# Optimization experiments

Measured on AMD Instinct MI355X. Metric: run time of the kernel, lower is better.

The kernel has to match this reference:

```python
import jax, jax.numpy as jnp
import numpy as np

DIM = 768
N_HEADS = 12
HEAD_DIM = DIM // N_HEADS
SCALE = 1.0 / (DIM ** 0.5)  # NOTE: module divides by sqrt(dim), not sqrt(head_dim)


def setup_inputs() -> dict:
    key = jax.random.key(0)
    ks = jax.random.split(key, 9)
    B, N = 16, 1024
    std = 1.0 / np.sqrt(DIM)
    inputs = jax.random.normal(ks[0], (B, N, DIM), dtype=jnp.float32)
    Wq = jax.random.normal(ks[1], (DIM, DIM), dtype=jnp.float32) * std
    bq = jax.random.normal(ks[2], (DIM,), dtype=jnp.float32) * std
    Wk = jax.random.normal(ks[3], (DIM, DIM), dtype=jnp.float32) * std
    bk = jax.random.normal(ks[4], (DIM,), dtype=jnp.float32) * std
    Wv = jax.random.normal(ks[5], (DIM, DIM), dtype=jnp.float32) * std
    bv = jax.random.normal(ks[6], (DIM,), dtype=jnp.float32) * std
    Wo = jax.random.normal(ks[7], (DIM, DIM), dtype=jnp.float32) * std
    bo = jax.random.normal(ks[8], (DIM,), dtype=jnp.float32) * std
    return {"inputs": inputs, "Wq": Wq, "bq": bq, "Wk": Wk, "bk": bk,
            "Wv": Wv, "bv": bv, "Wo": Wo, "bo": bo}


def _split_heads(x, B, N):
    # [B, N, DIM] -> [B, H, N, hd]
    return x.reshape(B, N, N_HEADS, HEAD_DIM).transpose(0, 2, 1, 3)


def reference(inputs, Wq, bq, Wk, bk, Wv, bv, Wo, bo):
    B, N, _ = inputs.shape
    q = _split_heads(inputs @ Wq + bq, B, N)
    k = _split_heads(inputs @ Wk + bk, B, N)
    v = _split_heads(inputs @ Wv + bv, B, N)
    scores = jnp.einsum('bhqd,bhkd->bhqk', q, k) * SCALE
    attn = jax.nn.softmax(scores, axis=-1)
    out = jnp.einsum('bhqk,bhkd->bhqd', attn, v)
    out = out.transpose(0, 2, 1, 3).reshape(B, N, DIM)
    return out @ Wo + bo
```

## Files before the change

### kernel.cpp

```cpp
#include <hip/hip_runtime.h>
#include <hip/hip_bf16.h>
#include <math.h>

#define DIM 768
#define NH 12
#define HD 64
#define BATCH 16
#define SEQ 1024
#define M_TOTAL (BATCH * SEQ)
#define MATE ((size_t)M_TOTAL * DIM)

typedef unsigned short ushort_t;
typedef __attribute__((ext_vector_type(8))) short short8;
typedef __attribute__((ext_vector_type(4))) float floatx4;

__device__ __constant__ float kScale = 0.03608439182435161f;

__device__ inline ushort_t f2b(float x) {
    __hip_bfloat16 h = __float2bfloat16(x);
    return __builtin_bit_cast(ushort_t, h);
}
__device__ inline float b2f_u32(unsigned int bits16) {
    union { unsigned int i; float f; } c;
    c.i = bits16 << 16;
    return c.f;
}
__device__ inline float b2f(ushort_t u) { return b2f_u32((unsigned int)u); }

__device__ __forceinline__ void gl2lds16(const ushort_t* g, ushort_t* l) {
    __builtin_amdgcn_global_load_lds(
        (__attribute__((address_space(1))) void*)g,
        (__attribute__((address_space(3))) void*)l, 16, 0, 0);
}

__global__ __launch_bounds__(256) void cvt_bf16_kernel(
    const float* __restrict__ X, ushort_t* __restrict__ Y, int n4)
{
    int i = blockIdx.x * 256 + threadIdx.x;
    if (i >= n4) return;
    float4 v = ((const float4*)X)[i];
    ushort4 o;
    o.x = f2b(v.x); o.y = f2b(v.y); o.z = f2b(v.z); o.w = f2b(v.w);
    ((ushort4*)Y)[i] = o;
}

__global__ __launch_bounds__(256) void transpose4_kernel(
    const float* __restrict__ W0, const float* __restrict__ W1,
    const float* __restrict__ W2, const float* __restrict__ W3,
    ushort_t* __restrict__ qkv_t, ushort_t* __restrict__ o_t)
{
    const int z = blockIdx.z;
    const float* W = (z == 0) ? W0 : (z == 1) ? W1 : (z == 2) ? W2 : W3;
    ushort_t* hi = (z < 3) ? qkv_t + (size_t)z * DIM * DIM : o_t;

    __shared__ float t[64][65];
    const int k0 = blockIdx.x * 64, n0 = blockIdx.y * 64;
    const int lr = threadIdx.x >> 2, lc = (threadIdx.x & 3) * 16;
    #pragma unroll
    for (int j = 0; j < 4; ++j) {
        float4 v = *(const float4*)&W[(size_t)(k0 + lr) * DIM + n0 + lc + j * 4];
        t[lr][lc + j * 4 + 0] = v.x;
        t[lr][lc + j * 4 + 1] = v.y;
        t[lr][lc + j * 4 + 2] = v.z;
        t[lr][lc + j * 4 + 3] = v.w;
    }
    __syncthreads();
    #pragma unroll
    for (int j = 0; j < 16; ++j)
        hi[(size_t)(n0 + lr) * DIM + k0 + lc + j] = f2b(t[lc + j][lr]);
}

__global__ __launch_bounds__(256) void bias_concat_kernel(
    const float* __restrict__ bq, const float* __restrict__ bk,
    const float* __restrict__ bv, float* __restrict__ ball)
{
    int i = blockIdx.x * 256 + threadIdx.x;
    if (i >= 3 * DIM) return;
    float v = (i < DIM) ? bq[i] : (i < 2 * DIM ? bk[i - DIM] : bv[i - 2 * DIM]);
    ball[i] = v;
}

template <int EPI>
__global__ __launch_bounds__(256) void mfma_gemm(
    const ushort_t* __restrict__ A, const ushort_t* __restrict__ Bhi,
    const float* __restrict__ bias, void* __restrict__ Cout)
{
    __shared__ ushort_t sA[128 * 32];
    __shared__ ushort_t sB[128 * 32];

    const int bid = blockIdx.x;
    const int xcd = bid & 7;
    const int o = bid >> 3;
    const int row0 = (xcd * 16 + (o & 15)) * 128;
    const int col0 = (o >> 4) * 128;

    const int tid = threadIdx.x;
    const int lane = tid & 63;
    const int wave = tid >> 6;
    const int wm = (wave & 1) * 64;
    const int wn = (wave >> 1) * 64;
    const int m16 = lane & 15;
    const int quad = lane >> 4;

    const int srow = lane >> 2;
    const int schunk = (lane & 3) * 8;

    const size_t aoff = (size_t)(row0 + wave * 32 + srow) * DIM + schunk;
    const size_t boff = (size_t)(col0 + wave * 32 + srow) * DIM + schunk;
    ushort_t* lA0 = sA + wave * 1024;
    ushort_t* lA1 = lA0 + 512;
    ushort_t* lB0 = sB + wave * 1024;
    ushort_t* lB1 = lB0 + 512;

    floatx4 acc[4][4];
    #pragma unroll
    for (int i = 0; i < 4; ++i)
        #pragma unroll
        for (int j = 0; j < 4; ++j)
            acc[i][j] = (floatx4){0.f, 0.f, 0.f, 0.f};

    for (int k0 = 0; k0 < DIM; k0 += 32) {
        __syncthreads();
        gl2lds16(A + aoff + k0, lA0);
        gl2lds16(A + aoff + (size_t)16 * DIM + k0, lA1);
        gl2lds16(Bhi + boff + k0, lB0);
        gl2lds16(Bhi + boff + (size_t)16 * DIM + k0, lB1);
        __syncthreads();

        short8 af[4], bh[4];
        #pragma unroll
        for (int i = 0; i < 4; ++i) {
            af[i] = *(const short8*)&sA[(wm + i * 16 + m16) * 32 + quad * 8];
            bh[i] = *(const short8*)&sB[(wn + i * 16 + m16) * 32 + quad * 8];
        }
        #pragma unroll
        for (int i = 0; i < 4; ++i)
            #pragma unroll
            for (int j = 0; j < 4; ++j)
                acc[i][j] = __builtin_amdgcn_mfma_f32_16x16x32_bf16(af[i], bh[j], acc[i][j], 0, 0, 0);
    }

    if (EPI == 0) {
        const int proj = col0 / DIM;
        const int rem0 = col0 % DIM;
        const float sc = (proj == 0) ? kScale : 1.0f;
        ushort_t* C = (ushort_t*)Cout + (size_t)proj * MATE;
        #pragma unroll
        for (int j = 0; j < 4; ++j) {
            const int coff = wn + j * 16 + m16;
            const int cc = rem0 + coff;
            const int h = cc >> 6, dd = cc & 63;
            const float bs = bias[col0 + coff];
            #pragma unroll
            for (int i = 0; i < 4; ++i)
                #pragma unroll
                for (int r = 0; r < 4; ++r) {
                    const int m = row0 + wm + i * 16 + quad * 4 + r;
                    const int bb = m >> 10, nn = m & 1023;
                    if (proj < 2) {
                        C[(((size_t)(bb * NH + h) * SEQ + nn) << 6) + dd] =
                            f2b((acc[i][j][r] + bs) * sc);
                    } else {
                        C[((((size_t)(bb * NH + h) << 6) + dd) << 10) + nn] =
                            f2b(acc[i][j][r] + bs);
                    }
                }
        }
    } else {
        float* C = (float*)Cout;
        #pragma unroll
        for (int j = 0; j < 4; ++j) {
            const int coff = wn + j * 16 + m16;
            const float bs = bias[col0 + coff];
            #pragma unroll
            for (int i = 0; i < 4; ++i)
                #pragma unroll
                for (int r = 0; r < 4; ++r) {
                    const int m = row0 + wm + i * 16 + quad * 4 + r;
                    C[(size_t)m * DIM + col0 + coff] = acc[i][j][r] + bs;
                }
        }
    }
}

#define APK 72
__global__ __launch_bounds__(256) void attn_kernel(
    const ushort_t* __restrict__ Q, const ushort_t* __restrict__ K,
    const ushort_t* __restrict__ Vt, ushort_t* __restrict__ Aout)
{
    __shared__ ushort_t Ks[64 * APK];
    __shared__ ushort_t Vs[64 * APK];
    __shared__ ushort_t Ps[128 * APK];

    const int bid = blockIdx.x;
    const int xcd = bid & 7;
    const int o = bid >> 3;
    const int bh = xcd * 24 + (o >> 3);
    const int q0 = (o & 7) * 128;

    const int tid = threadIdx.x;
    const int lane = tid & 63;
    const int wave = tid >> 6;
    const int wq = wave * 32;
    const int m16 = lane & 15;
    const int quad = lane >> 4;
    const size_t base  = (size_t)bh * SEQ * HD;
    const size_t baseT = (size_t)bh * HD * SEQ;

    const int sr = tid >> 2;
    const int sc = (tid & 3) * 16;

    short8 qf[2][2];
    #pragma unroll
    for (int f = 0; f < 2; ++f)
        #pragma unroll
        for (int kc = 0; kc < 2; ++kc)
            qf[f][kc] = *(const short8*)&Q[base +
                (size_t)(q0 + wq + f * 16 + m16) * HD + kc * 32 + quad * 8];

    floatx4 oacc[2][4];
    float lacc[2][4];
    #pragma unroll
    for (int f = 0; f < 2; ++f) {
        #pragma unroll
        for (int dt = 0; dt < 4; ++dt) oacc[f][dt] = (floatx4){0.f, 0.f, 0.f, 0.f};
        #pragma unroll
        for (int r = 0; r < 4; ++r) lacc[f][r] = 0.0f;
    }

    uint4 kv0 = *(const uint4*)&K[base + (size_t)sr * HD + sc];
    uint4 kv1 = *(const uint4*)&K[base + (size_t)sr * HD + sc + 8];
    uint4 vv0 = *(const uint4*)&Vt[baseT + (size_t)sr * SEQ + sc];
    uint4 vv1 = *(const uint4*)&Vt[baseT + (size_t)sr * SEQ + sc + 8];

    for (int kt = 0; kt < SEQ / 64; ++kt) {
        __syncthreads();
        *(uint4*)&Ks[sr * APK + sc] = kv0;
        *(uint4*)&Ks[sr * APK + sc + 8] = kv1;
        *(uint4*)&Vs[sr * APK + sc] = vv0;
        *(uint4*)&Vs[sr * APK + sc + 8] = vv1;
        __syncthreads();
        if (kt + 1 < SEQ / 64) {
            const int k1 = (kt + 1) * 64;
            kv0 = *(const uint4*)&K[base + (size_t)(k1 + sr) * HD + sc];
            kv1 = *(const uint4*)&K[base + (size_t)(k1 + sr) * HD + sc + 8];
            vv0 = *(const uint4*)&Vt[baseT + (size_t)sr * SEQ + k1 + sc];
            vv1 = *(const uint4*)&Vt[baseT + (size_t)sr * SEQ + k1 + sc + 8];
        }

        short8 kf[2][4];
        #pragma unroll
        for (int kc = 0; kc < 2; ++kc)
            #pragma unroll
            for (int t = 0; t < 4; ++t)
                kf[kc][t] = *(const short8*)&Ks[(t * 16 + m16) * APK + kc * 32 + quad * 8];
        floatx4 sacc[2][4];
        #pragma unroll
        for (int f = 0; f < 2; ++f)
            #pragma unroll
            for (int t = 0; t < 4; ++t)
                sacc[f][t] = (floatx4){0.f, 0.f, 0.f, 0.f};
        #pragma unroll
        for (int kc = 0; kc < 2; ++kc)
            #pragma unroll
            for (int f = 0; f < 2; ++f)
                #pragma unroll
                for (int t = 0; t < 4; ++t)
                    sacc[f][t] = __builtin_amdgcn_mfma_f32_16x16x32_bf16(
                        qf[f][kc], kf[kc][t], sacc[f][t], 0, 0, 0);

        #pragma unroll
        for (int f = 0; f < 2; ++f)
            #pragma unroll
            for (int r = 0; r < 4; ++r) {
                float rs = 0.0f;
                #pragma unroll
                for (int t = 0; t < 4; ++t) {
                    ushort_t u = f2b(__expf(sacc[f][t][r]));
                    Ps[(wq + f * 16 + quad * 4 + r) * APK + t * 16 + m16] = u;
                    rs += b2f(u);
                }
                lacc[f][r] += rs;
            }

        short8 vf[2][4];
        #pragma unroll
        for (int kc = 0; kc < 2; ++kc)
            #pragma unroll
            for (int dt = 0; dt < 4; ++dt)
                vf[kc][dt] = *(const short8*)&Vs[(dt * 16 + m16) * APK + kc * 32 + quad * 8];
        #pragma unroll
        for (int f = 0; f < 2; ++f) {
            #pragma unroll
            for (int kc = 0; kc < 2; ++kc) {
                short8 pf = *(const short8*)&Ps[(wq + f * 16 + m16) * APK + kc * 32 + quad * 8];
                #pragma unroll
                for (int dt = 0; dt < 4; ++dt)
                    oacc[f][dt] = __builtin_amdgcn_mfma_f32_16x16x32_bf16(
                        pf, vf[kc][dt], oacc[f][dt], 0, 0, 0);
            }
        }
    }

    float inv[2][4];
    #pragma unroll
    for (int f = 0; f < 2; ++f)
        #pragma unroll
        for (int r = 0; r < 4; ++r) {
            float l = lacc[f][r];
            l += __shfl_xor(l, 1);
            l += __shfl_xor(l, 2);
            l += __shfl_xor(l, 4);
            l += __shfl_xor(l, 8);
            inv[f][r] = 1.0f / l;
        }

    #pragma unroll
    for (int f = 0; f < 2; ++f)
        #pragma unroll
        for (int dt = 0; dt < 4; ++dt)
            #pragma unroll
            for (int r = 0; r < 4; ++r)
                Ps[(wq + f * 16 + quad * 4 + r) * APK + dt * 16 + m16] =
                    f2b(oacc[f][dt][r] * inv[f][r]);
    __syncthreads();

    const int b = bh / NH, h = bh % NH;
    const int orow = tid >> 1;
    const int oc = (tid & 1) * 32;
    const size_t row = (size_t)b * SEQ + q0 + orow;
    #pragma unroll
    for (int j = 0; j < 4; ++j) {
        uint4 ov = *(const uint4*)&Ps[orow * APK + oc + j * 8];
        *(uint4*)&Aout[row * DIM + h * HD + oc + j * 8] = ov;
    }
}

extern "C" void kernel_launch(void* const* d_in, const int* in_sizes, int n_in,
                              void* d_out, int out_size, void* d_ws, size_t ws_size,
                              hipStream_t stream)
{
    const float* X  = (const float*)d_in[0];
    const float* Wq = (const float*)d_in[1];
    const float* bq = (const float*)d_in[2];
    const float* Wk = (const float*)d_in[3];
    const float* bk = (const float*)d_in[4];
    const float* Wv = (const float*)d_in[5];
    const float* bv = (const float*)d_in[6];
    const float* Wo = (const float*)d_in[7];
    const float* bo = (const float*)d_in[8];

    ushort_t* qkv  = (ushort_t*)d_ws;
    ushort_t* abuf = qkv + 3 * MATE;
    ushort_t* xbf  = abuf + MATE;
    ushort_t* wqkv_t = xbf + MATE;
    ushort_t* wo_t   = wqkv_t + (size_t)3 * DIM * DIM;
    float* ball = (float*)(wo_t + (size_t)DIM * DIM);

    cvt_bf16_kernel<<<(int)(MATE / 4 + 255) / 256, 256, 0, stream>>>(X, xbf, (int)(MATE / 4));
    transpose4_kernel<<<dim3(DIM / 64, DIM / 64, 4), 256, 0, stream>>>(
        Wq, Wk, Wv, Wo, wqkv_t, wo_t);
    bias_concat_kernel<<<(3 * DIM + 255) / 256, 256, 0, stream>>>(bq, bk, bv, ball);

    mfma_gemm<0><<<dim3(18 * 128), 256, 0, stream>>>(xbf, wqkv_t, ball, qkv);

    attn_kernel<<<dim3((SEQ / 128) * BATCH * NH), 256, 0, stream>>>(
        qkv, qkv + MATE, qkv + 2 * MATE, abuf);

    mfma_gemm<1><<<dim3(6 * 128), 256, 0, stream>>>(abuf, wo_t, bo, d_out);
}
```

Measured before the change: 329.0 us.

## Triple-buffer GEMM LDS tiles with swizzled layout and a single barrier per step

The projection GEMM moves from a single-buffered LDS tile with two barriers per k-step to a 3-stage ring. It prefetches two tiles ahead, using vmcnt waits and one barrier per iteration. LDS rows get an XOR swizzle on the 8-element chunk index to cut bank conflicts on fragment reads, and MFMA sections are raised in wave priority. This aims to overlap global-to-LDS loads with MFMA work, at the cost of three times the shared memory, which may limit occupancy.

```diff
diff --git a/kernel.cpp b/kernel.cpp
--- a/kernel.cpp
+++ b/kernel.cpp
@@ -81,12 +81,12 @@
 }
 
 template <int EPI>
-__global__ __launch_bounds__(256) void mfma_gemm(
+__global__ __launch_bounds__(256, 3) void mfma_gemm(
     const ushort_t* __restrict__ A, const ushort_t* __restrict__ Bhi,
     const float* __restrict__ bias, void* __restrict__ Cout)
 {
-    __shared__ ushort_t sA[128 * 32];
-    __shared__ ushort_t sB[128 * 32];
+    __shared__ ushort_t sA[3 * 4096];
+    __shared__ ushort_t sB[3 * 4096];
 
     const int bid = blockIdx.x;
     const int xcd = bid & 7;
@@ -102,15 +102,26 @@
     const int m16 = lane & 15;
     const int quad = lane >> 4;
 
-    const int srow = lane >> 2;
-    const int schunk = (lane & 3) * 8;
-
-    const size_t aoff = (size_t)(row0 + wave * 32 + srow) * DIM + schunk;
-    const size_t boff = (size_t)(col0 + wave * 32 + srow) * DIM + schunk;
-    ushort_t* lA0 = sA + wave * 1024;
-    ushort_t* lA1 = lA0 + 512;
-    ushort_t* lB0 = sB + wave * 1024;
-    ushort_t* lB1 = lB0 + 512;
+    int offA[4], offB[4];
+    #pragma unroll
+    for (int i = 0; i < 4; ++i) {
+        const int ra = wm + i * 16 + m16;
+        offA[i] = ra * 32 + (quad ^ ((ra >> 1) & 3)) * 8;
+        const int rb = wn + i * 16 + m16;
+        offB[i] = rb * 32 + (quad ^ ((rb >> 1) & 3)) * 8;
+    }
+
+    size_t srcA[2], srcB[2];
+    int ldsoff[2];
+    #pragma unroll
+    for (int j = 0; j < 2; ++j) {
+        const int p = (wave * 2 + j) * 64 + lane;
+        const int row = p >> 2;
+        const int cg = (p & 3) ^ ((row >> 1) & 3);
+        srcA[j] = (size_t)(row0 + row) * DIM + cg * 8;
+        srcB[j] = (size_t)(col0 + row) * DIM + cg * 8;
+        ldsoff[j] = (wave * 2 + j) * 512;
+    }
 
     floatx4 acc[4][4];
     #pragma unroll
@@ -119,26 +130,54 @@
         for (int j = 0; j < 4; ++j)
             acc[i][j] = (floatx4){0.f, 0.f, 0.f, 0.f};
 
-    for (int k0 = 0; k0 < DIM; k0 += 32) {
-        __syncthreads();
-        gl2lds16(A + aoff + k0, lA0);
-        gl2lds16(A + aoff + (size_t)16 * DIM + k0, lA1);
-        gl2lds16(Bhi + boff + k0, lB0);
-        gl2lds16(Bhi + boff + (size_t)16 * DIM + k0, lB1);
-        __syncthreads();
-
-        short8 af[4], bh[4];
+    auto STAGE = [&](int sb, int kt) {
+        const int kk = kt * 32;
+        ushort_t* a = &sA[sb * 4096];
+        ushort_t* b = &sB[sb * 4096];
+        gl2lds16(A + srcA[0] + kk, a + ldsoff[0]);
+        gl2lds16(A + srcA[1] + kk, a + ldsoff[1]);
+        gl2lds16(Bhi + srcB[0] + kk, b + ldsoff[0]);
+        gl2lds16(Bhi + srcB[1] + kk, b + ldsoff[1]);
+    };
+    auto BODY = [&](int cb) {
+        const ushort_t* a = &sA[cb * 4096];
+        const ushort_t* b = &sB[cb * 4096];
+        short8 af[4], bf[4];
         #pragma unroll
         for (int i = 0; i < 4; ++i) {
-            af[i] = *(const short8*)&sA[(wm + i * 16 + m16) * 32 + quad * 8];
-            bh[i] = *(const short8*)&sB[(wn + i * 16 + m16) * 32 + quad * 8];
-        }
+            af[i] = *(const short8*)&a[offA[i]];
+            bf[i] = *(const short8*)&b[offB[i]];
+        }
+        __builtin_amdgcn_s_setprio(1);
         #pragma unroll
         for (int i = 0; i < 4; ++i)
             #pragma unroll
             for (int j = 0; j < 4; ++j)
-                acc[i][j] = __builtin_amdgcn_mfma_f32_16x16x32_bf16(af[i], bh[j], acc[i][j], 0, 0, 0);
-    }
+                acc[i][j] = __builtin_amdgcn_mfma_f32_16x16x32_bf16(af[i], bf[j], acc[i][j], 0, 0, 0);
+        __builtin_amdgcn_s_setprio(0);
+    };
+
+    STAGE(0, 0);
+    STAGE(1, 1);
+    asm volatile("s_waitcnt vmcnt(4)" ::: "memory");
+    __builtin_amdgcn_s_barrier();
+    __builtin_amdgcn_sched_barrier(0);
+
+    int bc = 0, bs = 2;
+    for (int t = 0; t < 22; ++t) {
+        STAGE(bs, t + 2);
+        BODY(bc);
+        asm volatile("s_waitcnt vmcnt(4)" ::: "memory");
+        __builtin_amdgcn_s_barrier();
+        __builtin_amdgcn_sched_barrier(0);
+        bc = (bc == 2) ? 0 : bc + 1;
+        bs = (bs == 2) ? 0 : bs + 1;
+    }
+    BODY(bc);
+    asm volatile("s_waitcnt vmcnt(0)" ::: "memory");
+    __builtin_amdgcn_s_barrier();
+    __builtin_amdgcn_sched_barrier(0);
+    BODY(2);
 
     if (EPI == 0) {
         const int proj = col0 / DIM;
@@ -150,7 +189,7 @@
             const int coff = wn + j * 16 + m16;
             const int cc = rem0 + coff;
             const int h = cc >> 6, dd = cc & 63;
-            const float bs = bias[col0 + coff];
+            const float bs2 = bias[col0 + coff];
             #pragma unroll
             for (int i = 0; i < 4; ++i)
                 #pragma unroll
@@ -159,10 +198,10 @@
                     const int bb = m >> 10, nn = m & 1023;
                     if (proj < 2) {
                         C[(((size_t)(bb * NH + h) * SEQ + nn) << 6) + dd] =
-                            f2b((acc[i][j][r] + bs) * sc);
+                            f2b((acc[i][j][r] + bs2) * sc);
                     } else {
                         C[((((size_t)(bb * NH + h) << 6) + dd) << 10) + nn] =
-                            f2b(acc[i][j][r] + bs);
+                            f2b(acc[i][j][r] + bs2);
                     }
                 }
         }
@@ -171,13 +210,13 @@
         #pragma unroll
         for (int j = 0; j < 4; ++j) {
             const int coff = wn + j * 16 + m16;
-            const float bs = bias[col0 + coff];
+            const float bs2 = bias[col0 + coff];
             #pragma unroll
             for (int i = 0; i < 4; ++i)
                 #pragma unroll
                 for (int r = 0; r < 4; ++r) {
                     const int m = row0 + wm + i * 16 + quad * 4 + r;
-                    C[(size_t)m * DIM + col0 + coff] = acc[i][j][r] + bs;
+                    C[(size_t)m * DIM + col0 + coff] = acc[i][j][r] + bs2;
                 }
         }
     }
```

Result: no change. 329.1 us (+0.0%).

## Rewrite projection GEMMs as 256x256 double-buffered, swizzled 8-wave pipelined kernel

Applied to the files above, without the earlier changes.

The QKV and output projection GEMMs move from 128x128 tiles with BK=32 and a sync-load-sync loop to 256x256 tiles with BK=64, 512 threads and double-buffered LDS. Global-to-LDS loads for the next K tiles are interleaved with the MFMA phases, and an XOR swizzle avoids LDS bank conflicts. This aims to raise arithmetic intensity and hide memory latency behind compute. In exchange it uses 128 KB of LDS per block and many accumulator registers, and the output GEMM launches only 192 blocks, which may underfill the GPU.

```diff
diff --git a/kernel.cpp b/kernel.cpp
--- a/kernel.cpp
+++ b/kernel.cpp
@@ -33,6 +33,12 @@
         (__attribute__((address_space(3))) void*)l, 16, 0, 0);
 }
 
+#define BAR() do { \
+    __builtin_amdgcn_sched_barrier(0); \
+    __builtin_amdgcn_s_barrier(); \
+    __builtin_amdgcn_sched_barrier(0); \
+} while (0)
+
 __global__ __launch_bounds__(256) void cvt_bf16_kernel(
     const float* __restrict__ X, ushort_t* __restrict__ Y, int n4)
 {
@@ -81,63 +87,115 @@
 }
 
 template <int EPI>
-__global__ __launch_bounds__(256) void mfma_gemm(
+__global__ __launch_bounds__(512, 2) void mfma_gemm(
     const ushort_t* __restrict__ A, const ushort_t* __restrict__ Bhi,
     const float* __restrict__ bias, void* __restrict__ Cout)
 {
-    __shared__ ushort_t sA[128 * 32];
-    __shared__ ushort_t sB[128 * 32];
+    constexpr int NT = 12;
+    __shared__ ushort_t smem[2 * 32768];
 
     const int bid = blockIdx.x;
     const int xcd = bid & 7;
     const int o = bid >> 3;
-    const int row0 = (xcd * 16 + (o & 15)) * 128;
-    const int col0 = (o >> 4) * 128;
+    const int row0 = (xcd * 8 + (o & 7)) * 256;
+    const int col0 = (o >> 3) * 256;
 
     const int tid = threadIdx.x;
     const int lane = tid & 63;
-    const int wave = tid >> 6;
-    const int wm = (wave & 1) * 64;
-    const int wn = (wave >> 1) * 64;
+    const int wv = tid >> 6;
+    const int wm = (wv >> 2) * 128;
+    const int wn = (wv & 3) * 64;
     const int m16 = lane & 15;
     const int quad = lane >> 4;
 
-    const int srow = lane >> 2;
-    const int schunk = (lane & 3) * 8;
-
-    const size_t aoff = (size_t)(row0 + wave * 32 + srow) * DIM + schunk;
-    const size_t boff = (size_t)(col0 + wave * 32 + srow) * DIM + schunk;
-    ushort_t* lA0 = sA + wave * 1024;
-    ushort_t* lA1 = lA0 + 512;
-    ushort_t* lB0 = sB + wave * 1024;
-    ushort_t* lB1 = lB0 + 512;
-
-    floatx4 acc[4][4];
-    #pragma unroll
-    for (int i = 0; i < 4; ++i)
+    size_t srcA[2], srcB[2];
+    int ldsoff[2];
+    #pragma unroll
+    for (int j = 0; j < 2; ++j) {
+        const int q = (wv * 2 + j) * 64 + lane;
+        const int r = q >> 3;
+        const int s = (q & 7) ^ (r & 7);
+        srcA[j] = (size_t)(row0 + r) * DIM + s * 8;
+        srcB[j] = (size_t)(col0 + r) * DIM + s * 8;
+        ldsoff[j] = (wv * 2 + j) * 512;
+    }
+
+    auto stageA = [&](int half, int kt, ushort_t* buf) {
+        const size_t hb = (size_t)half * 128 * DIM + (size_t)kt * 64;
+        ushort_t* d = buf + half * 8192;
+        gl2lds16(A + hb + srcA[0], d + ldsoff[0]);
+        gl2lds16(A + hb + srcA[1], d + ldsoff[1]);
+    };
+    auto stageB = [&](int half, int kt, ushort_t* buf) {
+        const size_t hb = (size_t)half * 128 * DIM + (size_t)kt * 64;
+        ushort_t* d = buf + 16384 + half * 8192;
+        gl2lds16(Bhi + hb + srcB[0], d + ldsoff[0]);
+        gl2lds16(Bhi + hb + srcB[1], d + ldsoff[1]);
+    };
+
+    floatx4 acc[8][4];
+    #pragma unroll
+    for (int i = 0; i < 8; ++i)
         #pragma unroll
         for (int j = 0; j < 4; ++j)
             acc[i][j] = (floatx4){0.f, 0.f, 0.f, 0.f};
 
-    for (int k0 = 0; k0 < DIM; k0 += 32) {
-        __syncthreads();
-        gl2lds16(A + aoff + k0, lA0);
-        gl2lds16(A + aoff + (size_t)16 * DIM + k0, lA1);
-        gl2lds16(Bhi + boff + k0, lB0);
-        gl2lds16(Bhi + boff + (size_t)16 * DIM + k0, lB1);
-        __syncthreads();
-
-        short8 af[4], bh[4];
-        #pragma unroll
-        for (int i = 0; i < 4; ++i) {
-            af[i] = *(const short8*)&sA[(wm + i * 16 + m16) * 32 + quad * 8];
-            bh[i] = *(const short8*)&sB[(wn + i * 16 + m16) * 32 + quad * 8];
-        }
-        #pragma unroll
-        for (int i = 0; i < 4; ++i)
-            #pragma unroll
-            for (int j = 0; j < 4; ++j)
-                acc[i][j] = __builtin_amdgcn_mfma_f32_16x16x32_bf16(af[i], bh[j], acc[i][j], 0, 0, 0);
+    stageA(0, 0, smem); stageA(1, 0, smem);
+    stageB(0, 0, smem); stageB(1, 0, smem);
+    stageB(0, 1, smem + 32768); stageB(1, 1, smem + 32768);
+    asm volatile("s_waitcnt vmcnt(4)" ::: "memory");
+    BAR();
+
+    for (int t = 0; t < NT; ++t) {
+        ushort_t* bc = smem + (t & 1) * 32768;
+        ushort_t* bn = smem + ((t & 1) ^ 1) * 32768;
+        const ushort_t* a = bc;
+        const ushort_t* b = bc + 16384;
+        short8 bf[4][2];
+        #pragma unroll
+        for (int p = 0; p < 4; ++p) {
+            short8 af[2][2];
+            if (p == 0) {
+                #pragma unroll
+                for (int n = 0; n < 4; ++n)
+                    #pragma unroll
+                    for (int s = 0; s < 2; ++s) {
+                        const int r = wn + n * 16 + m16;
+                        bf[n][s] = *(const short8*)&b[r * 64 + ((s * 4 + quad) ^ (r & 7)) * 8];
+                    }
+            }
+            #pragma unroll
+            for (int i = 0; i < 2; ++i)
+                #pragma unroll
+                for (int s = 0; s < 2; ++s) {
+                    const int r = wm + (p * 2 + i) * 16 + m16;
+                    af[i][s] = *(const short8*)&a[r * 64 + ((s * 4 + quad) ^ (r & 7)) * 8];
+                }
+            if (p == 0 && t + 1 < NT) stageA(0, t + 1, bn);
+            if (p == 1) {
+                if (t + 1 < NT) stageA(1, t + 1, bn);
+                if (t + 2 < NT) stageB(0, t + 2, bc);
+            }
+            if (p == 2 && t + 2 < NT) stageB(1, t + 2, bc);
+            BAR();
+            asm volatile("s_waitcnt lgkmcnt(0)" ::: "memory");
+            __builtin_amdgcn_sched_barrier(0);
+            __builtin_amdgcn_s_setprio(1);
+            #pragma unroll
+            for (int i = 0; i < 2; ++i)
+                #pragma unroll
+                for (int n = 0; n < 4; ++n)
+                    #pragma unroll
+                    for (int s = 0; s < 2; ++s)
+                        acc[p * 2 + i][n] = __builtin_amdgcn_mfma_f32_16x16x32_bf16(
+                            af[i][s], bf[n][s], acc[p * 2 + i][n], 0, 0, 0);
+            __builtin_amdgcn_s_setprio(0);
+            if (p == 3) {
+                if (t < NT - 2) asm volatile("s_waitcnt vmcnt(4)" ::: "memory");
+                else            asm volatile("s_waitcnt vmcnt(0)" ::: "memory");
+            }
+            BAR();
+        }
     }
 
     if (EPI == 0) {
@@ -146,38 +204,38 @@
         const float sc = (proj == 0) ? kScale : 1.0f;
         ushort_t* C = (ushort_t*)Cout + (size_t)proj * MATE;
         #pragma unroll
-        for (int j = 0; j < 4; ++j) {
-            const int coff = wn + j * 16 + m16;
+        for (int n = 0; n < 4; ++n) {
+            const int coff = wn + n * 16 + m16;
             const int cc = rem0 + coff;
             const int h = cc >> 6, dd = cc & 63;
-            const float bs = bias[col0 + coff];
-            #pragma unroll
-            for (int i = 0; i < 4; ++i)
+            const float bs2 = bias[col0 + coff];
+            #pragma unroll
+            for (int m = 0; m < 8; ++m)
                 #pragma unroll
                 for (int r = 0; r < 4; ++r) {
-                    const int m = row0 + wm + i * 16 + quad * 4 + r;
-                    const int bb = m >> 10, nn = m & 1023;
+                    const int mm = row0 + wm + m * 16 + quad * 4 + r;
+                    const int bb = mm >> 10, nn = mm & 1023;
                     if (proj < 2) {
                         C[(((size_t)(bb * NH + h) * SEQ + nn) << 6) + dd] =
-                            f2b((acc[i][j][r] + bs) * sc);
+                            f2b((acc[m][n][r] + bs2) * sc);
                     } else {
                         C[((((size_t)(bb * NH + h) << 6) + dd) << 10) + nn] =
-                            f2b(acc[i][j][r] + bs);
+                            f2b(acc[m][n][r] + bs2);
                     }
                 }
         }
     } else {
         float* C = (float*)Cout;
         #pragma unroll
-        for (int j = 0; j < 4; ++j) {
-            const int coff = wn + j * 16 + m16;
-            const float bs = bias[col0 + coff];
-            #pragma unroll
-            for (int i = 0; i < 4; ++i)
+        for (int n = 0; n < 4; ++n) {
+            const int coff = wn + n * 16 + m16;
+            const float bs2 = bias[col0 + coff];
+            #pragma unroll
+            for (int m = 0; m < 8; ++m)
                 #pragma unroll
                 for (int r = 0; r < 4; ++r) {
-                    const int m = row0 + wm + i * 16 + quad * 4 + r;
-                    C[(size_t)m * DIM + col0 + coff] = acc[i][j][r] + bs;
+                    const int mm = row0 + wm + m * 16 + quad * 4 + r;
+                    C[(size_t)mm * DIM + col0 + coff] = acc[m][n][r] + bs2;
                 }
         }
     }
@@ -362,10 +420,10 @@
         Wq, Wk, Wv, Wo, wqkv_t, wo_t);
     bias_concat_kernel<<<(3 * DIM + 255) / 256, 256, 0, stream>>>(bq, bk, bv, ball);
 
-    mfma_gemm<0><<<dim3(18 * 128), 256, 0, stream>>>(xbf, wqkv_t, ball, qkv);
+    mfma_gemm<0><<<dim3(8 * 72), 512, 0, stream>>>(xbf, wqkv_t, ball, qkv);
 
     attn_kernel<<<dim3((SEQ / 128) * BATCH * NH), 256, 0, stream>>>(
         qkv, qkv + MATE, qkv + 2 * MATE, abuf);
 
-    mfma_gemm<1><<<dim3(6 * 128), 256, 0, stream>>>(abuf, wo_t, bo, d_out);
-}
+    mfma_gemm<1><<<dim3(8 * 24), 512, 0, stream>>>(abuf, wo_t, bo, d_out);
+}
```

After: 335.9 us. +2.1%, slower.

## Merge prep kernels into one launch and deepen GEMM K-tile with swizzled LDS

Applied to the files above, without the earlier changes.

The three preprocessing kernels (fp32-to-bf16 conversion of X, weight transpose/convert, bias concat) become a single launch whose block index selects the task, removing two kernel launches. The MFMA GEMM now loads a K-tile of 64 instead of 32 per barrier pair. This halves the number of __syncthreads per GEMM and does more MFMA work per load phase. LDS reads use an XOR swizzle to avoid bank conflicts. The cost is doubled LDS usage per block, which may lower occupancy.

```diff
diff --git a/kernel.cpp b/kernel.cpp
--- a/kernel.cpp
+++ b/kernel.cpp
@@ -33,51 +33,49 @@
         (__attribute__((address_space(3))) void*)l, 16, 0, 0);
 }
 
-__global__ __launch_bounds__(256) void cvt_bf16_kernel(
-    const float* __restrict__ X, ushort_t* __restrict__ Y, int n4)
-{
-    int i = blockIdx.x * 256 + threadIdx.x;
-    if (i >= n4) return;
-    float4 v = ((const float4*)X)[i];
-    ushort4 o;
-    o.x = f2b(v.x); o.y = f2b(v.y); o.z = f2b(v.z); o.w = f2b(v.w);
-    ((ushort4*)Y)[i] = o;
-}
-
-__global__ __launch_bounds__(256) void transpose4_kernel(
+#define NCVT 12288
+__global__ __launch_bounds__(256) void prep_kernel(
+    const float* __restrict__ X, ushort_t* __restrict__ Y,
     const float* __restrict__ W0, const float* __restrict__ W1,
     const float* __restrict__ W2, const float* __restrict__ W3,
-    ushort_t* __restrict__ qkv_t, ushort_t* __restrict__ o_t)
-{
-    const int z = blockIdx.z;
-    const float* W = (z == 0) ? W0 : (z == 1) ? W1 : (z == 2) ? W2 : W3;
-    ushort_t* hi = (z < 3) ? qkv_t + (size_t)z * DIM * DIM : o_t;
-
-    __shared__ float t[64][65];
-    const int k0 = blockIdx.x * 64, n0 = blockIdx.y * 64;
-    const int lr = threadIdx.x >> 2, lc = (threadIdx.x & 3) * 16;
-    #pragma unroll
-    for (int j = 0; j < 4; ++j) {
-        float4 v = *(const float4*)&W[(size_t)(k0 + lr) * DIM + n0 + lc + j * 4];
-        t[lr][lc + j * 4 + 0] = v.x;
-        t[lr][lc + j * 4 + 1] = v.y;
-        t[lr][lc + j * 4 + 2] = v.z;
-        t[lr][lc + j * 4 + 3] = v.w;
-    }
-    __syncthreads();
-    #pragma unroll
-    for (int j = 0; j < 16; ++j)
-        hi[(size_t)(n0 + lr) * DIM + k0 + lc + j] = f2b(t[lc + j][lr]);
-}
-
-__global__ __launch_bounds__(256) void bias_concat_kernel(
+    ushort_t* __restrict__ qkv_t, ushort_t* __restrict__ o_t,
     const float* __restrict__ bq, const float* __restrict__ bk,
     const float* __restrict__ bv, float* __restrict__ ball)
 {
-    int i = blockIdx.x * 256 + threadIdx.x;
+    __shared__ float t[64][65];
+    const int b = blockIdx.x;
+    if (b < NCVT) {
+        const int i = b * 256 + threadIdx.x;
+        float4 v = ((const float4*)X)[i];
+        ushort4 o;
+        o.x = f2b(v.x); o.y = f2b(v.y); o.z = f2b(v.z); o.w = f2b(v.w);
+        ((ushort4*)Y)[i] = o;
+        return;
+    }
+    if (b < NCVT + 576) {
+        const int tt = b - NCVT;
+        const int z = tt / 144, rem = tt % 144;
+        const float* W = (z == 0) ? W0 : (z == 1) ? W1 : (z == 2) ? W2 : W3;
+        ushort_t* hi = (z < 3) ? qkv_t + (size_t)z * DIM * DIM : o_t;
+        const int k0 = (rem / 12) * 64, n0 = (rem % 12) * 64;
+        const int lr = threadIdx.x >> 2, lc = (threadIdx.x & 3) * 16;
+        #pragma unroll
+        for (int j = 0; j < 4; ++j) {
+            float4 v = *(const float4*)&W[(size_t)(k0 + lr) * DIM + n0 + lc + j * 4];
+            t[lr][lc + j * 4 + 0] = v.x;
+            t[lr][lc + j * 4 + 1] = v.y;
+            t[lr][lc + j * 4 + 2] = v.z;
+            t[lr][lc + j * 4 + 3] = v.w;
+        }
+        __syncthreads();
+        #pragma unroll
+        for (int j = 0; j < 16; ++j)
+            hi[(size_t)(n0 + lr) * DIM + k0 + lc + j] = f2b(t[lc + j][lr]);
+        return;
+    }
+    const int i = (b - NCVT - 576) * 256 + threadIdx.x;
     if (i >= 3 * DIM) return;
-    float v = (i < DIM) ? bq[i] : (i < 2 * DIM ? bk[i - DIM] : bv[i - 2 * DIM]);
-    ball[i] = v;
+    ball[i] = (i < DIM) ? bq[i] : (i < 2 * DIM ? bk[i - DIM] : bv[i - 2 * DIM]);
 }
 
 template <int EPI>
@@ -85,8 +83,8 @@
     const ushort_t* __restrict__ A, const ushort_t* __restrict__ Bhi,
     const float* __restrict__ bias, void* __restrict__ Cout)
 {
-    __shared__ ushort_t sA[128 * 32];
-    __shared__ ushort_t sB[128 * 32];
+    __shared__ ushort_t sA[128 * 64];
+    __shared__ ushort_t sB[128 * 64];
 
     const int bid = blockIdx.x;
     const int xcd = bid & 7;
@@ -102,15 +100,17 @@
     const int m16 = lane & 15;
     const int quad = lane >> 4;
 
-    const int srow = lane >> 2;
-    const int schunk = (lane & 3) * 8;
-
-    const size_t aoff = (size_t)(row0 + wave * 32 + srow) * DIM + schunk;
-    const size_t boff = (size_t)(col0 + wave * 32 + srow) * DIM + schunk;
-    ushort_t* lA0 = sA + wave * 1024;
-    ushort_t* lA1 = lA0 + 512;
-    ushort_t* lB0 = sB + wave * 1024;
-    ushort_t* lB1 = lB0 + 512;
+    size_t srcA[4], srcB[4];
+    int dstoff[4];
+    #pragma unroll
+    for (int j = 0; j < 4; ++j) {
+        const int q = wave * 256 + j * 64 + lane;
+        const int r = q >> 3;
+        const int ls = (q & 7) ^ (r & 7);
+        srcA[j] = (size_t)(row0 + r) * DIM + ls * 8;
+        srcB[j] = (size_t)(col0 + r) * DIM + ls * 8;
+        dstoff[j] = (wave * 256 + j * 64) * 8;
+    }
 
     floatx4 acc[4][4];
     #pragma unroll
@@ -119,25 +119,32 @@
         for (int j = 0; j < 4; ++j)
             acc[i][j] = (floatx4){0.f, 0.f, 0.f, 0.f};
 
-    for (int k0 = 0; k0 < DIM; k0 += 32) {
-        __syncthreads();
-        gl2lds16(A + aoff + k0, lA0);
-        gl2lds16(A + aoff + (size_t)16 * DIM + k0, lA1);
-        gl2lds16(Bhi + boff + k0, lB0);
-        gl2lds16(Bhi + boff + (size_t)16 * DIM + k0, lB1);
-        __syncthreads();
-
-        short8 af[4], bh[4];
-        #pragma unroll
-        for (int i = 0; i < 4; ++i) {
-            af[i] = *(const short8*)&sA[(wm + i * 16 + m16) * 32 + quad * 8];
-            bh[i] = *(const short8*)&sB[(wn + i * 16 + m16) * 32 + quad * 8];
-        }
-        #pragma unroll
-        for (int i = 0; i < 4; ++i)
-            #pragma unroll
-            for (int j = 0; j < 4; ++j)
-                acc[i][j] = __builtin_amdgcn_mfma_f32_16x16x32_bf16(af[i], bh[j], acc[i][j], 0, 0, 0);
+    for (int t = 0; t < DIM / 64; ++t) {
+        const int kk = t * 64;
+        __syncthreads();
+        #pragma unroll
+        for (int j = 0; j < 4; ++j) {
+            gl2lds16(A + srcA[j] + kk, sA + dstoff[j]);
+            gl2lds16(Bhi + srcB[j] + kk, sB + dstoff[j]);
+        }
+        __syncthreads();
+
+        #pragma unroll
+        for (int s = 0; s < 2; ++s) {
+            short8 af[4], bf[4];
+            #pragma unroll
+            for (int i = 0; i < 4; ++i) {
+                const int ra = wm + i * 16 + m16;
+                af[i] = *(const short8*)&sA[ra * 64 + (((s * 4 + quad) ^ (ra & 7)) * 8)];
+                const int rb = wn + i * 16 + m16;
+                bf[i] = *(const short8*)&sB[rb * 64 + (((s * 4 + quad) ^ (rb & 7)) * 8)];
+            }
+            #pragma unroll
+            for (int i = 0; i < 4; ++i)
+                #pragma unroll
+                for (int j = 0; j < 4; ++j)
+                    acc[i][j] = __builtin_amdgcn_mfma_f32_16x16x32_bf16(af[i], bf[j], acc[i][j], 0, 0, 0);
+        }
     }
 
     if (EPI == 0) {
@@ -357,10 +364,8 @@
     ushort_t* wo_t   = wqkv_t + (size_t)3 * DIM * DIM;
     float* ball = (float*)(wo_t + (size_t)DIM * DIM);
 
-    cvt_bf16_kernel<<<(int)(MATE / 4 + 255) / 256, 256, 0, stream>>>(X, xbf, (int)(MATE / 4));
-    transpose4_kernel<<<dim3(DIM / 64, DIM / 64, 4), 256, 0, stream>>>(
-        Wq, Wk, Wv, Wo, wqkv_t, wo_t);
-    bias_concat_kernel<<<(3 * DIM + 255) / 256, 256, 0, stream>>>(bq, bk, bv, ball);
+    prep_kernel<<<dim3(NCVT + 576 + 9), 256, 0, stream>>>(
+        X, xbf, Wq, Wk, Wv, Wo, wqkv_t, wo_t, bq, bk, bv, ball);
 
     mfma_gemm<0><<<dim3(18 * 128), 256, 0, stream>>>(xbf, wqkv_t, ball, qkv);
 
```

Result: slower. 339.4 us (+3.1%).
